# Optimization experiments

Measured on AMD Instinct MI355X. Metric: run time of the kernel, lower is better.

## Reference

```python
import jax, jax.numpy as jnp
import numpy as np

N_NODES = 200000
N_EDGES = 1600000
N_GRAPHS = 4096  # B*T = 256*16
FEATS = [5, 64, 128, 128]
H = 128


def setup_inputs() -> dict:
    key = jax.random.key(0)
    ks = jax.random.split(key, 32)
    inp = {
        "x": jax.random.normal(ks[0], (N_NODES, FEATS[0]), jnp.float32),
        "edge_attr": jax.random.uniform(ks[1], (N_EDGES,), jnp.float32),
        "edge_index": jax.random.randint(ks[2], (2, N_EDGES), 0, N_NODES),
        "batch_labels": jnp.sort(jax.random.randint(ks[3], (N_NODES,), 0, N_GRAPHS)),
        "label_map": jnp.arange(N_GRAPHS).reshape(256, 16),
    }
    ki = 4
    # GraphConv layers: self weight, neighbor weight, bias
    for li, (a, b) in enumerate(zip(FEATS[:-1], FEATS[1:])):
        s = (2.0 / a) ** 0.5
        inp[f"w_self{li}"] = jax.random.normal(ks[ki], (a, b), jnp.float32) * s; ki += 1
        inp[f"w_nei{li}"] = jax.random.normal(ks[ki], (a, b), jnp.float32) * s; ki += 1
        inp[f"b{li}"] = jnp.zeros((b,), jnp.float32)
    # GRU layers (PyTorch layout: W_ih [3H, in], W_hh [3H, H])
    for l in range(2):
        d_in = FEATS[-1] if l == 0 else H
        s = (1.0 / H) ** 0.5
        inp[f"wih{l}"] = jax.random.uniform(ks[ki], (3 * H, d_in), jnp.float32, -s, s); ki += 1
        inp[f"whh{l}"] = jax.random.uniform(ks[ki], (3 * H, H), jnp.float32, -s, s); ki += 1
        inp[f"bih{l}"] = jnp.zeros((3 * H,), jnp.float32)
        inp[f"bhh{l}"] = jnp.zeros((3 * H,), jnp.float32)
    inp["w_dec"] = jax.random.normal(ks[ki], (H, 1), jnp.float32) * (1.0 / H) ** 0.5; ki += 1
    inp["b_dec"] = jnp.zeros((1,), jnp.float32)
    return inp


def _gru_layer(seq, wih, whh, bih, bhh):
    # seq: [B, T, D] -> out [B, T, H], h_last [B, H]
    Hd = whh.shape[1]
    x_proj = seq @ wih.T + bih  # [B, T, 3H], precompute input projections

    def step(h_prev, xt):
        gh = h_prev @ whh.T + bhh
        xr, xz, xn = jnp.split(xt, 3, axis=-1)
        hr, hz, hn = jnp.split(gh, 3, axis=-1)
        r = jax.nn.sigmoid(xr + hr)
        z = jax.nn.sigmoid(xz + hz)
        n = jnp.tanh(xn + r * hn)
        h_new = (1.0 - z) * n + z * h_prev
        return h_new, h_new

    h0 = jnp.zeros((seq.shape[0], Hd), seq.dtype)
    h_last, outs = jax.lax.scan(step, h0, jnp.swapaxes(x_proj, 0, 1))
    return jnp.swapaxes(outs, 0, 1), h_last


def reference(x, edge_attr, w_self0, w_nei0, b0, w_self1, w_nei1, b1,
              w_self2, w_nei2, b2, wih0, whh0, bih0, bhh0, wih1, whh1,
              bih1, bhh1, w_dec, b_dec, edge_index, batch_labels, label_map):
    src, dst = edge_index[0], edge_index[1]
    n = x.shape[0]

    def conv(h, ws, wn, bb):
        # message = edge_weight * (W_nei h_src); aggregate by sum onto dst
        hn = h @ wn
        msg = hn[src] * edge_attr[:, None]  # [E, out]
        agg = jax.ops.segment_sum(msg, dst, num_segments=n)
        return jax.nn.relu(h @ ws + agg + bb)

    h = conv(x, w_self0, w_nei0, b0)
    h = conv(h, w_self1, w_nei1, b1)
    h = conv(h, w_self2, w_nei2, b2)

    # global_mean_pool over batch_labels
    sums = jax.ops.segment_sum(h, batch_labels, num_segments=N_GRAPHS)
    cnt = jax.ops.segment_sum(jnp.ones((n,), h.dtype), batch_labels, num_segments=N_GRAPHS)
    pooled = sums / jnp.maximum(cnt, 1.0)[:, None]  # [G, H]

    # group pooled graph embeddings into padded sequences [B, T, H]
    seq = pooled[label_map]

    o1, _ = _gru_layer(seq, wih0, whh0, bih0, bhh0)
    o2, h2 = _gru_layer(o1, wih1, whh1, bih1, bhh1)

    predictions = jax.nn.sigmoid(o2 @ w_dec + b_dec).squeeze(-1)  # [B, T]
    final_prediction = jax.nn.sigmoid(h2 @ w_dec + b_dec)  # [B, 1]
    return predictions, final_prediction
```

## Files before the change

### kernel.cpp

```cpp
#include <hip/hip_runtime.h>
#include <cmath>

typedef __attribute__((ext_vector_type(8))) short short8b;
typedef __attribute__((ext_vector_type(8))) unsigned short ushort8b;
typedef __attribute__((ext_vector_type(4))) float floatx4;

__device__ __forceinline__ float sigm(float x) { return 1.0f / (1.0f + expf(-x)); }

__device__ __forceinline__ unsigned short f2bf(float f) {
    unsigned u = __float_as_uint(f);
    unsigned r = (u + 0x7FFFu + ((u >> 16) & 1u)) >> 16;
    return (unsigned short)r;
}
__device__ __forceinline__ float bf2f(unsigned short b) {
    return __uint_as_float(((unsigned)b) << 16);
}

__global__ __launch_bounds__(512)
void bucket_hist(const int* __restrict__ dst, int* __restrict__ bcnt, int nE, int nBuck)
{
    __shared__ int h[512];
    const int t = threadIdx.x;
    h[t] = 0;
    __syncthreads();
    for (int i = blockIdx.x * 512 + t; i < nE; i += gridDim.x * 512)
        atomicAdd(&h[dst[i] >> 9], 1);
    __syncthreads();
    if (t < nBuck && h[t]) atomicAdd(&bcnt[t], h[t]);
}

__global__ __launch_bounds__(256)
void scan_blocks(const int* __restrict__ in, int* __restrict__ out,
                 int* __restrict__ bsum, int n)
{
    __shared__ int sh[256];
    int base = blockIdx.x * 1024;
    int t = threadIdx.x;
    int v[4];
    int s = 0;
    #pragma unroll
    for (int q = 0; q < 4; ++q) {
        int idx = base + t * 4 + q;
        v[q] = (idx < n) ? in[idx] : 0;
        s += v[q];
    }
    sh[t] = s;
    __syncthreads();
    for (int off = 1; off < 256; off <<= 1) {
        int x = (t >= off) ? sh[t - off] : 0;
        __syncthreads();
        sh[t] += x;
        __syncthreads();
    }
    int run = (t == 0) ? 0 : sh[t - 1];
    #pragma unroll
    for (int q = 0; q < 4; ++q) {
        int idx = base + t * 4 + q;
        if (idx < n) out[idx] = run;
        run += v[q];
    }
    if (t == 255 && bsum) bsum[blockIdx.x] = sh[255];
}

__global__ __launch_bounds__(512)
void bucket_scatter(const int* __restrict__ src, const int* __restrict__ dst,
                    const float* __restrict__ ea, int* __restrict__ bcur,
                    uint2* __restrict__ recs, int nE)
{
    __shared__ int hcnt[512];
    __shared__ int hbase[512];
    const int t = threadIdx.x;
    const int base = blockIdx.x * 8192;
    hcnt[t] = 0;
    __syncthreads();
    int eb[16], rank[16], dloc[16];
    #pragma unroll
    for (int q = 0; q < 16; ++q) {
        int e = base + q * 512 + t;
        if (e < nE) {
            int d = dst[e];
            eb[q] = d >> 9;
            dloc[q] = d & 511;
            rank[q] = atomicAdd(&hcnt[eb[q]], 1);
        }
    }
    __syncthreads();
    hbase[t] = hcnt[t] ? atomicAdd(&bcur[t], hcnt[t]) : 0;
    __syncthreads();
    #pragma unroll
    for (int q = 0; q < 16; ++q) {
        int e = base + q * 512 + t;
        if (e < nE) {
            int wq2 = __float2int_rn(ea[e] * 16383.f);
            uint2 r;
            r.x = (unsigned)((src[e] << 14) | wq2);
            r.y = (unsigned)dloc[q];
            recs[hbase[eb[q]] + rank[q]] = r;
        }
    }
}

__global__ __launch_bounds__(512)
void bucket_finalize(const uint2* __restrict__ recs, const int* __restrict__ boff,
                     int* __restrict__ rowptr, int* __restrict__ csr,
                     int nN, int nE, int nBuck)
{
    __shared__ int cnt[512];
    __shared__ int sc[512];
    __shared__ int cur[512];
    const int b = blockIdx.x;
    const int t = threadIdx.x;
    const int rbase = boff[b];
    const int rend  = (b + 1 < nBuck) ? boff[b + 1] : nE;
    const int rcnt  = rend - rbase;
    const int node0 = b << 9;
    const int nodes = min(512, nN - node0);
    cnt[t] = 0;
    __syncthreads();
    for (int i = t; i < rcnt; i += 512) atomicAdd(&cnt[recs[rbase + i].y], 1);
    __syncthreads();
    sc[t] = cnt[t];
    __syncthreads();
    for (int off = 1; off < 512; off <<= 1) {
        int v = (t >= off) ? sc[t - off] : 0;
        __syncthreads();
        sc[t] += v;
        __syncthreads();
    }
    int excl = (t == 0) ? 0 : sc[t - 1];
    if (t < nodes) rowptr[node0 + t] = rbase + excl;
    cur[t] = excl;
    __syncthreads();
    for (int i = t; i < rcnt; i += 512) {
        uint2 r = recs[rbase + i];
        int p = atomicAdd(&cur[r.y], 1);
        csr[rbase + p] = (int)r.x;
    }
}

__global__ __launch_bounds__(256)
void agg5_kernel(const float* __restrict__ x, const int* __restrict__ rowptr,
                 const int* __restrict__ csr, float* __restrict__ agg, int nN, int nE)
{
    int n = blockIdx.x * blockDim.x + threadIdx.x;
    if (n >= nN) return;
    int e0 = rowptr[n];
    int e1 = (n + 1 < nN) ? rowptr[n + 1] : nE;
    float a[5] = {0.f, 0.f, 0.f, 0.f, 0.f};
    for (int e = e0; e < e1; ++e) {
        int v = csr[e];
        int s = ((unsigned)v) >> 14;
        float w = (float)(v & 16383) * (1.f / 16383.f);
        const float* xr = x + (size_t)s * 5;
        #pragma unroll
        for (int f = 0; f < 5; ++f) a[f] += w * xr[f];
    }
    float* ar = agg + (size_t)n * 5;
    #pragma unroll
    for (int f = 0; f < 5; ++f) ar[f] = a[f];
}

template<int D>
__global__ __launch_bounds__(256)
void aggD_bf16(const unsigned short* __restrict__ h, const int* __restrict__ rowptr,
               const int* __restrict__ csr, unsigned short* __restrict__ agg,
               int nN, int nE)
{
    constexpr int TPN = D / 8;
    int gid = blockIdx.x * blockDim.x + threadIdx.x;
    int c = gid & (TPN - 1);
    int n = gid / TPN;
    if (n >= nN) return;
    int e0 = rowptr[n];
    int e1 = (n + 1 < nN) ? rowptr[n + 1] : nE;
    float acc[8] = {0.f, 0.f, 0.f, 0.f, 0.f, 0.f, 0.f, 0.f};
    int e = e0;
    for (; e + 3 < e1; e += 4) {
        int v0 = csr[e], v1 = csr[e + 1], v2 = csr[e + 2], v3 = csr[e + 3];
        const ushort8b h0 = *(const ushort8b*)(h + (size_t)(((unsigned)v0) >> 14) * D + c * 8);
        const ushort8b h1 = *(const ushort8b*)(h + (size_t)(((unsigned)v1) >> 14) * D + c * 8);
        const ushort8b h2 = *(const ushort8b*)(h + (size_t)(((unsigned)v2) >> 14) * D + c * 8);
        const ushort8b h3 = *(const ushort8b*)(h + (size_t)(((unsigned)v3) >> 14) * D + c * 8);
        float w0 = (float)(v0 & 16383) * (1.f / 16383.f);
        float w1 = (float)(v1 & 16383) * (1.f / 16383.f);
        float w2 = (float)(v2 & 16383) * (1.f / 16383.f);
        float w3 = (float)(v3 & 16383) * (1.f / 16383.f);
        #pragma unroll
        for (int q = 0; q < 8; ++q) {
            acc[q] += w0 * bf2f(h0[q]);
            acc[q] += w1 * bf2f(h1[q]);
            acc[q] += w2 * bf2f(h2[q]);
            acc[q] += w3 * bf2f(h3[q]);
        }
    }
    for (; e < e1; ++e) {
        int v = csr[e];
        int s = ((unsigned)v) >> 14;
        float w = (float)(v & 16383) * (1.f / 16383.f);
        const ushort8b hv = *(const ushort8b*)(h + (size_t)s * D + c * 8);
        #pragma unroll
        for (int q = 0; q < 8; ++q) acc[q] += w * bf2f(hv[q]);
    }
    ushort8b o;
    #pragma unroll
    for (int q = 0; q < 8; ++q) o[q] = f2bf(acc[q]);
    *(ushort8b*)(agg + (size_t)n * D + c * 8) = o;
}

template<int DIN, int DOUT>
__global__ __launch_bounds__(512)
void conv_mm(const float* __restrict__ h, const float* __restrict__ agg,
             const float* __restrict__ ws, const float* __restrict__ wn,
             const float* __restrict__ bias, unsigned short* __restrict__ out, int nN)
{
    __shared__ __align__(16) float s_w[2 * DIN * DOUT];
    __shared__ __align__(16) float s_b[DOUT];
    for (int i = threadIdx.x; i < DIN * DOUT; i += 512) {
        s_w[i] = ws[i];
        s_w[DIN * DOUT + i] = wn[i];
    }
    for (int i = threadIdx.x; i < DOUT; i += 512) s_b[i] = bias[i];
    __syncthreads();

    constexpr int TPN = DOUT / 4;
    constexpr int HALF = 512 / TPN;
    constexpr int NPASS = HALF * 2;
    const int jj = (threadIdx.x % TPN) * 4;
    const int nsub = threadIdx.x / TPN;

    for (int base = blockIdx.x * NPASS; base < nN; base += gridDim.x * NPASS) {
        int n0 = base + nsub;
        int n1 = base + nsub + HALF;
        bool v0 = n0 < nN, v1 = n1 < nN;
        int n0c = v0 ? n0 : nN - 1;
        int n1c = v1 ? n1 : nN - 1;

        float acc0[4], acc1[4];
        #pragma unroll
        for (int q = 0; q < 4; ++q) { acc0[q] = s_b[jj + q]; acc1[q] = s_b[jj + q]; }

        const float* p0 = h + (size_t)n0c * DIN;
        const float* p1 = h + (size_t)n1c * DIN;
        const float* a0 = agg + (size_t)n0c * DIN;
        const float* a1 = agg + (size_t)n1c * DIN;

        for (int k = 0; k < DIN; ++k) {
            float xs0 = p0[k], xs1 = p1[k];
            const float4 w4 = *(const float4*)(s_w + (size_t)k * DOUT + jj);
            acc0[0] += xs0 * w4.x; acc0[1] += xs0 * w4.y;
            acc0[2] += xs0 * w4.z; acc0[3] += xs0 * w4.w;
            acc1[0] += xs1 * w4.x; acc1[1] += xs1 * w4.y;
            acc1[2] += xs1 * w4.z; acc1[3] += xs1 * w4.w;
        }
        for (int k = 0; k < DIN; ++k) {
            float xs0 = a0[k], xs1 = a1[k];
            const float4 w4 = *(const float4*)(s_w + (size_t)(DIN + k) * DOUT + jj);
            acc0[0] += xs0 * w4.x; acc0[1] += xs0 * w4.y;
            acc0[2] += xs0 * w4.z; acc0[3] += xs0 * w4.w;
            acc1[0] += xs1 * w4.x; acc1[1] += xs1 * w4.y;
            acc1[2] += xs1 * w4.z; acc1[3] += xs1 * w4.w;
        }
        if (v0) {
            ushort4 o;
            o.x = f2bf(fmaxf(acc0[0], 0.f)); o.y = f2bf(fmaxf(acc0[1], 0.f));
            o.z = f2bf(fmaxf(acc0[2], 0.f)); o.w = f2bf(fmaxf(acc0[3], 0.f));
            *(ushort4*)(out + (size_t)n0 * DOUT + jj) = o;
        }
        if (v1) {
            ushort4 o;
            o.x = f2bf(fmaxf(acc1[0], 0.f)); o.y = f2bf(fmaxf(acc1[1], 0.f));
            o.z = f2bf(fmaxf(acc1[2], 0.f)); o.w = f2bf(fmaxf(acc1[3], 0.f));
            *(ushort4*)(out + (size_t)n1 * DOUT + jj) = o;
        }
    }
}

template<int DIN>
__global__ __launch_bounds__(256)
void prep_w(const float* __restrict__ ws, const float* __restrict__ wn,
            unsigned short* __restrict__ wt)
{
    constexpr int KC = 2 * DIN;
    int idx = blockIdx.x * 256 + threadIdx.x;
    if (idx >= 128 * KC) return;
    int col = idx / KC, k = idx % KC;
    float v = (k < DIN) ? ws[(size_t)k * 128 + col] : wn[(size_t)(k - DIN) * 128 + col];
    wt[(size_t)col * KC + k] = f2bf(v);
}

__global__ __launch_bounds__(256)
void prep_gru(const float* __restrict__ wih0, const float* __restrict__ whh0,
              const float* __restrict__ wih1, const float* __restrict__ whh1,
              unsigned short* __restrict__ wtx, unsigned short* __restrict__ wth)
{
    int i = blockIdx.x * 256 + threadIdx.x;
    if (i >= 384 * 128) return;
    wtx[i]             = f2bf(wih0[i]);
    wtx[384 * 128 + i] = f2bf(wih1[i]);
    wth[i]             = f2bf(whh0[i]);
    wth[384 * 128 + i] = f2bf(whh1[i]);
}

template<int DIN, bool POOL>
__global__ __launch_bounds__(256)
void conv_mfma(const unsigned short* __restrict__ h, const unsigned short* __restrict__ agg,
               const unsigned short* __restrict__ wt,
               const float* __restrict__ bias, unsigned short* __restrict__ out,
               const int* __restrict__ bl, float* __restrict__ sums, int nN)
{
    constexpr int KC = 2 * DIN;
    constexpr int NPANEL = KC / 64;
    constexpr int LDK = 72;
    constexpr int SMEM_BYTES = POOL ? 33280 : 27648;
    __shared__ __align__(16) unsigned char smem[SMEM_BYTES];
    unsigned short* sA = (unsigned short*)smem;
    unsigned short* sB = (unsigned short*)(smem + 9216);

    const int tid  = threadIdx.x;
    const int lane = tid & 63;
    const int w    = tid >> 6;
    const int nb   = (w >> 1) * 32;
    const int cb   = (w & 1) * 64;
    const int r15  = lane & 15;
    const int k8   = (lane >> 4) * 8;
    const int tile0 = blockIdx.x * 64;

    const floatx4 zero4 = {0.f, 0.f, 0.f, 0.f};
    floatx4 acc[2][4];
    #pragma unroll
    for (int m = 0; m < 2; ++m)
        #pragma unroll
        for (int n = 0; n < 4; ++n) acc[m][n] = zero4;

    for (int kp = 0; kp < NPANEL; ++kp) {
        const int kbase = kp * 64;
        const unsigned short* M = (kbase < DIN) ? h : agg;
        const int koff = (kbase < DIN) ? kbase : (kbase - DIN);
        #pragma unroll
        for (int r = 0; r < 2; ++r) {
            int f = tid + r * 256;
            int node = f >> 3, kq = f & 7;
            *(ushort8b*)(&sA[node * LDK + kq * 8]) =
                *(const ushort8b*)(M + (size_t)(tile0 + node) * DIN + koff + kq * 8);
        }
        #pragma unroll
        for (int r = 0; r < 4; ++r) {
            int f = tid + r * 256;
            int col = f >> 3, kq = f & 7;
            *(ushort8b*)(&sB[col * LDK + kq * 8]) =
                *(const ushort8b*)(wt + (size_t)col * KC + kbase + kq * 8);
        }
        __syncthreads();
        #pragma unroll
        for (int ks = 0; ks < 2; ++ks) {
            const int kk = ks * 32 + k8;
            short8b a0 = *(const short8b*)(&sA[(nb + r15) * LDK + kk]);
            short8b a1 = *(const short8b*)(&sA[(nb + 16 + r15) * LDK + kk]);
            #pragma unroll
            for (int n = 0; n < 4; ++n) {
                short8b b = *(const short8b*)(&sB[(cb + n * 16 + r15) * LDK + kk]);
                acc[0][n] = __builtin_amdgcn_mfma_f32_16x16x32_bf16(a0, b, acc[0][n], 0, 0, 0);
                acc[1][n] = __builtin_amdgcn_mfma_f32_16x16x32_bf16(a1, b, acc[1][n], 0, 0, 0);
            }
        }
        __syncthreads();
    }

    const int row4 = (lane >> 4) * 4;
    if constexpr (POOL) {
        float* s_out = (float*)smem;
        int*   s_gl  = (int*)(smem + 33024);
        #pragma unroll
        for (int n = 0; n < 4; ++n) {
            const int col = cb + n * 16 + r15;
            const float bv = bias[col];
            #pragma unroll
            for (int m = 0; m < 2; ++m) {
                #pragma unroll
                for (int j = 0; j < 4; ++j) {
                    int row = nb + m * 16 + row4 + j;
                    s_out[row * 129 + col] = fmaxf(acc[m][n][j] + bv, 0.f);
                }
            }
        }
        if (tid < 64) s_gl[tid] = bl[tile0 + tid];
        __syncthreads();
        {
            const int col  = tid & 127;
            const int r0   = (tid >> 7) * 32;
            float run = 0.f;
            int gprev = s_gl[r0];
            for (int r = r0; r < r0 + 32; ++r) {
                int g = s_gl[r];
                float v = s_out[r * 129 + col];
                if (g != gprev) {
                    unsafeAtomicAdd(&sums[(size_t)gprev * 128 + col], run);
                    run = v;
                    gprev = g;
                } else {
                    run += v;
                }
            }
            unsafeAtomicAdd(&sums[(size_t)gprev * 128 + col], run);
        }
    } else {
        #pragma unroll
        for (int n = 0; n < 4; ++n) {
            const int col = cb + n * 16 + r15;
            const float bv = bias[col];
            #pragma unroll
            for (int m = 0; m < 2; ++m) {
                #pragma unroll
                for (int j = 0; j < 4; ++j) {
                    int node = tile0 + nb + m * 16 + row4 + j;
                    out[(size_t)node * 128 + col] = f2bf(fmaxf(acc[m][n][j] + bv, 0.f));
                }
            }
        }
    }
}

__global__ __launch_bounds__(256)
void cnt_bs(const int* __restrict__ bl, float* __restrict__ cnt, int nN, int nG)
{
    int g = blockIdx.x * blockDim.x + threadIdx.x;
    if (g >= nG) return;
    int lo = 0, hi = nN;
    while (lo < hi) { int mid = (lo + hi) >> 1; if (bl[mid] < g) lo = mid + 1; else hi = mid; }
    int s = lo;
    hi = nN;
    while (lo < hi) { int mid = (lo + hi) >> 1; if (bl[mid] < g + 1) lo = mid + 1; else hi = mid; }
    cnt[g] = (float)(lo - s);
}

__global__ __launch_bounds__(256)
void xproj_kernel(const float* __restrict__ sums, const float* __restrict__ cnt,
                  const int* __restrict__ lmap, const unsigned short* __restrict__ wx0,
                  const float* __restrict__ bih0, float* __restrict__ xp, int nRows)
{
    __shared__ __align__(16) unsigned short s_a[32 * 136];
    __shared__ float s_b[384];
    const int tid  = threadIdx.x;
    const int lane = tid & 63;
    const int w    = tid >> 6;
    const int r15  = lane & 15;
    const int k8   = (lane >> 4) * 8;
    const int row4 = (lane >> 4) * 4;
    const int base = blockIdx.x * 32;

    for (int i = tid; i < 32 * 128; i += 256) {
        int row = i >> 7, j = i & 127;
        int g = lmap[base + row];
        float v = sums[(size_t)g * 128 + j] / fmaxf(cnt[g], 1.f);
        s_a[row * 136 + j] = f2bf(v);
    }
    for (int i = tid; i < 384; i += 256) s_b[i] = bih0[i];
    __syncthreads();

    const int rt = (w & 1) * 16;
    const int cg = (w >> 1) * 192;
    const floatx4 zero4 = {0.f, 0.f, 0.f, 0.f};
    floatx4 acc[12];
    #pragma unroll
    for (int ct = 0; ct < 12; ++ct) acc[ct] = zero4;

    #pragma unroll
    for (int kk = 0; kk < 4; ++kk) {
        short8b a = *(const short8b*)(&s_a[(rt + r15) * 136 + kk * 32 + k8]);
        #pragma unroll
        for (int ct = 0; ct < 12; ++ct) {
            int col = cg + ct * 16 + r15;
            short8b b = *(const short8b*)(wx0 + (size_t)col * 128 + kk * 32 + k8);
            acc[ct] = __builtin_amdgcn_mfma_f32_16x16x32_bf16(a, b, acc[ct], 0, 0, 0);
        }
    }
    #pragma unroll
    for (int ct = 0; ct < 12; ++ct) {
        int col = cg + ct * 16 + r15;
        float bv = s_b[col];
        #pragma unroll
        for (int j = 0; j < 4; ++j) {
            int R = base + rt + row4 + j;
            xp[(size_t)R * 384 + col] = acc[ct][j] + bv;
        }
    }
}

__global__ __launch_bounds__(384)
void gru_rec(const float* __restrict__ xp0,
             const unsigned short* __restrict__ wgx,
             const unsigned short* __restrict__ wgh,
             const float* __restrict__ bhh0, const float* __restrict__ bih1,
             const float* __restrict__ bhh1,
             const float* __restrict__ wdec, const float* __restrict__ bdec,
             float* __restrict__ out, int nG)
{
    constexpr int SLD = 136;
    __shared__ float s_xp[16 * 384];
    __shared__ __align__(16) unsigned short s_o[16 * SLD];
    __shared__ __align__(16) unsigned short s_hb[128];
    __shared__ float s_hf[128];
    __shared__ float s_gh[384];
    __shared__ float s_bhh[2][384];
    __shared__ float s_bih1[384];
    __shared__ float s_wdec[128];

    const int b    = blockIdx.x;
    const int tid  = threadIdx.x;
    const int lane = tid & 63;
    const int w    = tid >> 6;
    const int r15  = lane & 15;
    const int k8   = (lane >> 4) * 8;
    const int row4 = (lane >> 4) * 4;
    const int cbase = w * 64;
    const floatx4 zero4 = {0.f, 0.f, 0.f, 0.f};

    for (int i = tid; i < 16 * 384; i += 384)
        s_xp[i] = xp0[(size_t)b * 16 * 384 + i];
    s_bhh[0][tid] = bhh0[tid];
    s_bhh[1][tid] = bhh1[tid];
    s_bih1[tid]   = bih1[tid];
    if (tid < 128) { s_wdec[tid] = wdec[tid]; s_hf[tid] = 0.f; s_hb[tid] = 0; }

    short8b bf[4][4];
    {
        const unsigned short* W = wgh;
        #pragma unroll
        for (int ct = 0; ct < 4; ++ct) {
            int col = cbase + ct * 16 + r15;
            #pragma unroll
            for (int kk = 0; kk < 4; ++kk)
                bf[ct][kk] = *(const short8b*)(W + (size_t)col * 128 + kk * 32 + k8);
        }
    }
    __syncthreads();

    for (int t = 0; t < 16; ++t) {
        floatx4 acc[4] = {zero4, zero4, zero4, zero4};
        #pragma unroll
        for (int kk = 0; kk < 4; ++kk) {
            short8b a = *(const short8b*)(&s_hb[kk * 32 + k8]);
            #pragma unroll
            for (int ct = 0; ct < 4; ++ct)
                acc[ct] = __builtin_amdgcn_mfma_f32_16x16x32_bf16(a, bf[ct][kk], acc[ct], 0, 0, 0);
        }
        if (lane < 16) {
            #pragma unroll
            for (int ct = 0; ct < 4; ++ct) {
                int col = cbase + ct * 16 + lane;
                s_gh[col] = acc[ct][0] + s_bhh[0][col];
            }
        }
        __syncthreads();
        if (tid < 128) {
            const float* xr = &s_xp[t * 384];
            float r = sigm(xr[tid] + s_gh[tid]);
            float z = sigm(xr[128 + tid] + s_gh[128 + tid]);
            float n = tanhf(xr[256 + tid] + r * s_gh[256 + tid]);
            float hv = (1.f - z) * n + z * s_hf[tid];
            s_hf[tid] = hv;
            unsigned short hb = f2bf(hv);
            s_hb[tid] = hb;
            s_o[t * SLD + tid] = hb;
        }
        __syncthreads();
    }

    {
        const unsigned short* W1 = wgx + (size_t)384 * 128;
        #pragma unroll
        for (int ct = 0; ct < 4; ++ct) {
            int col = cbase + ct * 16 + r15;
            #pragma unroll
            for (int kk = 0; kk < 4; ++kk)
                bf[ct][kk] = *(const short8b*)(W1 + (size_t)col * 128 + kk * 32 + k8);
        }
        floatx4 acc[4] = {zero4, zero4, zero4, zero4};
        #pragma unroll
        for (int kk = 0; kk < 4; ++kk) {
            short8b a = *(const short8b*)(&s_o[r15 * SLD + kk * 32 + k8]);
            #pragma unroll
            for (int ct = 0; ct < 4; ++ct)
                acc[ct] = __builtin_amdgcn_mfma_f32_16x16x32_bf16(a, bf[ct][kk], acc[ct], 0, 0, 0);
        }
        #pragma unroll
        for (int ct = 0; ct < 4; ++ct) {
            int col = cbase + ct * 16 + r15;
            float bv = s_bih1[col];
            #pragma unroll
            for (int j = 0; j < 4; ++j) {
                int t = row4 + j;
                s_xp[t * 384 + col] = acc[ct][j] + bv;
            }
        }
    }
    {
        const unsigned short* W = wgh + (size_t)384 * 128;
        #pragma unroll
        for (int ct = 0; ct < 4; ++ct) {
            int col = cbase + ct * 16 + r15;
            #pragma unroll
            for (int kk = 0; kk < 4; ++kk)
                bf[ct][kk] = *(const short8b*)(W + (size_t)col * 128 + kk * 32 + k8);
        }
    }
    if (tid < 128) { s_hf[tid] = 0.f; s_hb[tid] = 0; }
    __syncthreads();

    for (int t = 0; t < 16; ++t) {
        floatx4 acc[4] = {zero4, zero4, zero4, zero4};
        #pragma unroll
        for (int kk = 0; kk < 4; ++kk) {
            short8b a = *(const short8b*)(&s_hb[kk * 32 + k8]);
            #pragma unroll
            for (int ct = 0; ct < 4; ++ct)
                acc[ct] = __builtin_amdgcn_mfma_f32_16x16x32_bf16(a, bf[ct][kk], acc[ct], 0, 0, 0);
        }
        if (lane < 16) {
            #pragma unroll
            for (int ct = 0; ct < 4; ++ct) {
                int col = cbase + ct * 16 + lane;
                s_gh[col] = acc[ct][0] + s_bhh[1][col];
            }
        }
        __syncthreads();
        if (tid < 128) {
            const float* xr = &s_xp[t * 384];
            float r = sigm(xr[tid] + s_gh[tid]);
            float z = sigm(xr[128 + tid] + s_gh[128 + tid]);
            float n = tanhf(xr[256 + tid] + r * s_gh[256 + tid]);
            float hv = (1.f - z) * n + z * s_hf[tid];
            s_hf[tid] = hv;
            unsigned short hb = f2bf(hv);
            s_hb[tid] = hb;
            s_o[t * SLD + tid] = hb;
        }
        __syncthreads();
    }

    if (tid < 16) {
        float acc = bdec[0];
        const unsigned short* row = &s_o[tid * SLD];
        #pragma unroll 16
        for (int k = 0; k < 128; ++k) acc += bf2f(row[k]) * s_wdec[k];
        float p = sigm(acc);
        out[b * 16 + tid] = p;
        if (tid == 15) out[nG + b] = p;
    }
}

extern "C" void kernel_launch(void* const* d_in, const int* in_sizes, int n_in,
                              void* d_out, int out_size, void* d_ws, size_t ws_size,
                              hipStream_t stream)
{
    const float* x    = (const float*)d_in[0];
    const float* ea   = (const float*)d_in[1];
    const int*   ei   = (const int*)d_in[2];
    const int*   bl   = (const int*)d_in[3];
    const int*   lmap = (const int*)d_in[4];
    const float* ws0 = (const float*)d_in[5];
    const float* wn0 = (const float*)d_in[6];
    const float* b0  = (const float*)d_in[7];
    const float* ws1 = (const float*)d_in[8];
    const float* wn1 = (const float*)d_in[9];
    const float* b1  = (const float*)d_in[10];
    const float* ws2 = (const float*)d_in[11];
    const float* wn2 = (const float*)d_in[12];
    const float* b2  = (const float*)d_in[13];
    const float* wih0 = (const float*)d_in[14];
    const float* whh0 = (const float*)d_in[15];
    const float* bih0 = (const float*)d_in[16];
    const float* bhh0 = (const float*)d_in[17];
    const float* wih1 = (const float*)d_in[18];
    const float* whh1 = (const float*)d_in[19];
    const float* bih1 = (const float*)d_in[20];
    const float* bhh1 = (const float*)d_in[21];
    const float* wdec = (const float*)d_in[22];
    const float* bdec = (const float*)d_in[23];
    float* out = (float*)d_out;

    const int nN = in_sizes[0] / 5;
    const int nE = in_sizes[1];
    const int nG = in_sizes[4];
    const int B  = nG / 16;
    const int nBuck = (nN + 511) >> 9;

    const int* src = ei;
    const int* dst = ei + nE;

    unsigned short* R0   = (unsigned short*)d_ws;
    unsigned short* R1   = R0 + (size_t)nN * 64;
    unsigned short* R2   = R1 + (size_t)nN * 64;
    unsigned short* agg128b = R0;
    float* agg5 = (float*)(R2 + (size_t)nN * 128);
    float* sums = agg5 + (size_t)nN * 5;
    float* cnt  = sums + (size_t)nG * 128;
    int* rowptr = (int*)(cnt + nG);
    int* bcnt   = rowptr + nN;
    int* boff   = bcnt + 512;
    int* bcur   = boff + 512;
    uint2* recs = (uint2*)(bcur + 512);
    int* csr    = (int*)(recs + nE);
    unsigned short* wt1 = (unsigned short*)(csr + nE);
    unsigned short* wt2 = wt1 + 128 * 128;
    unsigned short* wgx = wt2 + 128 * 256;
    unsigned short* wgh = wgx + 2 * 384 * 128;
    float* xp0 = (float*)(wgh + 2 * 384 * 128);

    hipMemsetAsync(bcnt, 0, 512 * sizeof(int), stream);
    bucket_hist<<<256, 512, 0, stream>>>(dst, bcnt, nE, nBuck);
    scan_blocks<<<1, 256, 0, stream>>>(bcnt, boff, nullptr, nBuck);
    hipMemcpyAsync(bcur, boff, nBuck * sizeof(int), hipMemcpyDeviceToDevice, stream);
    bucket_scatter<<<(nE + 8191) / 8192, 512, 0, stream>>>(src, dst, ea, bcur, recs, nE);
    bucket_finalize<<<nBuck, 512, 0, stream>>>(recs, boff, rowptr, csr, nN, nE, nBuck);

    prep_w<64><<<(128 * 128 + 255) / 256, 256, 0, stream>>>(ws1, wn1, wt1);
    prep_w<128><<<(128 * 256 + 255) / 256, 256, 0, stream>>>(ws2, wn2, wt2);
    prep_gru<<<(384 * 128 + 255) / 256, 256, 0, stream>>>(wih0, whh0, wih1, whh1, wgx, wgh);

    agg5_kernel<<<(nN + 255) / 256, 256, 0, stream>>>(x, rowptr, csr, agg5, nN, nE);
    conv_mm<5, 64><<<512, 512, 0, stream>>>(x, agg5, ws0, wn0, b0, R0, nN);

    aggD_bf16<64><<<(nN * 8 + 255) / 256, 256, 0, stream>>>(R0, rowptr, csr, R1, nN, nE);
    conv_mfma<64, false><<<nN / 64, 256, 0, stream>>>(R0, R1, wt1, b1, R2, nullptr, nullptr, nN);

    aggD_bf16<128><<<(nN * 16 + 255) / 256, 256, 0, stream>>>(R2, rowptr, csr, agg128b, nN, nE);
    hipMemsetAsync(sums, 0, (size_t)nG * 128 * sizeof(float), stream);
    cnt_bs<<<(nG + 255) / 256, 256, 0, stream>>>(bl, cnt, nN, nG);
    conv_mfma<128, true><<<nN / 64, 256, 0, stream>>>(R2, agg128b, wt2, b2, nullptr, bl, sums, nN);

    xproj_kernel<<<nG / 32, 256, 0, stream>>>(sums, cnt, lmap, wgx, bih0, xp0, nG);
    gru_rec<<<B, 384, 0, stream>>>(xp0, wgx, wgh, bhh0, bih1, bhh1, wdec, bdec, out, nG);
}
```

Baseline: 306.6 us.

## Fuse neighbor aggregation into MFMA conv kernel via shared-memory tile

The separate aggD_bf16 gather kernels are removed. Each conv block now aggregates its own 64 nodes' neighbor features into a shared-memory tile and feeds the agg half of the K dimension to the MFMAs straight from that tile. This avoids writing and re-reading the aggregated bf16 matrix through global memory and saves two kernel launches. In exchange, shared memory per block grows and the latency-bound gather now sits inside the GEMM kernel, which may reduce occupancy and overlap.

```diff
diff --git a/kernel.cpp b/kernel.cpp
--- a/kernel.cpp
+++ b/kernel.cpp
@@ -160,53 +160,6 @@
     for (int f = 0; f < 5; ++f) ar[f] = a[f];
 }
 
-template<int D>
-__global__ __launch_bounds__(256)
-void aggD_bf16(const unsigned short* __restrict__ h, const int* __restrict__ rowptr,
-               const int* __restrict__ csr, unsigned short* __restrict__ agg,
-               int nN, int nE)
-{
-    constexpr int TPN = D / 8;
-    int gid = blockIdx.x * blockDim.x + threadIdx.x;
-    int c = gid & (TPN - 1);
-    int n = gid / TPN;
-    if (n >= nN) return;
-    int e0 = rowptr[n];
-    int e1 = (n + 1 < nN) ? rowptr[n + 1] : nE;
-    float acc[8] = {0.f, 0.f, 0.f, 0.f, 0.f, 0.f, 0.f, 0.f};
-    int e = e0;
-    for (; e + 3 < e1; e += 4) {
-        int v0 = csr[e], v1 = csr[e + 1], v2 = csr[e + 2], v3 = csr[e + 3];
-        const ushort8b h0 = *(const ushort8b*)(h + (size_t)(((unsigned)v0) >> 14) * D + c * 8);
-        const ushort8b h1 = *(const ushort8b*)(h + (size_t)(((unsigned)v1) >> 14) * D + c * 8);
-        const ushort8b h2 = *(const ushort8b*)(h + (size_t)(((unsigned)v2) >> 14) * D + c * 8);
-        const ushort8b h3 = *(const ushort8b*)(h + (size_t)(((unsigned)v3) >> 14) * D + c * 8);
-        float w0 = (float)(v0 & 16383) * (1.f / 16383.f);
-        float w1 = (float)(v1 & 16383) * (1.f / 16383.f);
-        float w2 = (float)(v2 & 16383) * (1.f / 16383.f);
-        float w3 = (float)(v3 & 16383) * (1.f / 16383.f);
-        #pragma unroll
-        for (int q = 0; q < 8; ++q) {
-            acc[q] += w0 * bf2f(h0[q]);
-            acc[q] += w1 * bf2f(h1[q]);
-            acc[q] += w2 * bf2f(h2[q]);
-            acc[q] += w3 * bf2f(h3[q]);
-        }
-    }
-    for (; e < e1; ++e) {
-        int v = csr[e];
-        int s = ((unsigned)v) >> 14;
-        float w = (float)(v & 16383) * (1.f / 16383.f);
-        const ushort8b hv = *(const ushort8b*)(h + (size_t)s * D + c * 8);
-        #pragma unroll
-        for (int q = 0; q < 8; ++q) acc[q] += w * bf2f(hv[q]);
-    }
-    ushort8b o;
-    #pragma unroll
-    for (int q = 0; q < 8; ++q) o[q] = f2bf(acc[q]);
-    *(ushort8b*)(agg + (size_t)n * D + c * 8) = o;
-}
-
 template<int DIN, int DOUT>
 __global__ __launch_bounds__(512)
 void conv_mm(const float* __restrict__ h, const float* __restrict__ agg,
@@ -303,18 +256,23 @@
 
 template<int DIN, bool POOL>
 __global__ __launch_bounds__(256)
-void conv_mfma(const unsigned short* __restrict__ h, const unsigned short* __restrict__ agg,
-               const unsigned short* __restrict__ wt,
-               const float* __restrict__ bias, unsigned short* __restrict__ out,
-               const int* __restrict__ bl, float* __restrict__ sums, int nN)
+void conv_fused(const unsigned short* __restrict__ h,
+                const int* __restrict__ rowptr, const int* __restrict__ csr,
+                const unsigned short* __restrict__ wt,
+                const float* __restrict__ bias, unsigned short* __restrict__ out,
+                const int* __restrict__ bl, float* __restrict__ sums,
+                int nN, int nE)
 {
     constexpr int KC = 2 * DIN;
     constexpr int NPANEL = KC / 64;
     constexpr int LDK = 72;
-    constexpr int SMEM_BYTES = POOL ? 33280 : 27648;
+    constexpr int ALD = DIN + 8;
+    constexpr int BASE_BYTES = 9216 + 18432;
+    constexpr int SMEM_BYTES = BASE_BYTES + 64 * ALD * 2;
     __shared__ __align__(16) unsigned char smem[SMEM_BYTES];
-    unsigned short* sA = (unsigned short*)smem;
-    unsigned short* sB = (unsigned short*)(smem + 9216);
+    unsigned short* sA   = (unsigned short*)smem;
+    unsigned short* sB   = (unsigned short*)(smem + 9216);
+    unsigned short* sAgg = (unsigned short*)(smem + BASE_BYTES);
 
     const int tid  = threadIdx.x;
     const int lane = tid & 63;
@@ -325,6 +283,53 @@
     const int k8   = (lane >> 4) * 8;
     const int tile0 = blockIdx.x * 64;
 
+    {
+        constexpr int TPN = DIN / 8;
+        constexpr int GRP = 256 / TPN;
+        constexpr int NPT = 64 / GRP;
+        const int c  = tid & (TPN - 1);
+        const int n0 = tid / TPN;
+        #pragma unroll
+        for (int it = 0; it < NPT; ++it) {
+            int node = n0 + it * GRP;
+            int gn = tile0 + node;
+            int e0 = rowptr[gn];
+            int e1 = (gn + 1 < nN) ? rowptr[gn + 1] : nE;
+            float acc[8] = {0.f, 0.f, 0.f, 0.f, 0.f, 0.f, 0.f, 0.f};
+            int e = e0;
+            for (; e + 3 < e1; e += 4) {
+                int v0 = csr[e], v1 = csr[e + 1], v2 = csr[e + 2], v3 = csr[e + 3];
+                const ushort8b h0 = *(const ushort8b*)(h + (size_t)(((unsigned)v0) >> 14) * DIN + c * 8);
+                const ushort8b h1 = *(const ushort8b*)(h + (size_t)(((unsigned)v1) >> 14) * DIN + c * 8);
+                const ushort8b h2 = *(const ushort8b*)(h + (size_t)(((unsigned)v2) >> 14) * DIN + c * 8);
+                const ushort8b h3 = *(const ushort8b*)(h + (size_t)(((unsigned)v3) >> 14) * DIN + c * 8);
+                float w0 = (float)(v0 & 16383) * (1.f / 16383.f);
+                float w1 = (float)(v1 & 16383) * (1.f / 16383.f);
+                float w2 = (float)(v2 & 16383) * (1.f / 16383.f);
+                float w3 = (float)(v3 & 16383) * (1.f / 16383.f);
+                #pragma unroll
+                for (int q = 0; q < 8; ++q) {
+                    acc[q] += w0 * bf2f(h0[q]);
+                    acc[q] += w1 * bf2f(h1[q]);
+                    acc[q] += w2 * bf2f(h2[q]);
+                    acc[q] += w3 * bf2f(h3[q]);
+                }
+            }
+            for (; e < e1; ++e) {
+                int v = csr[e];
+                float wv = (float)(v & 16383) * (1.f / 16383.f);
+                const ushort8b hv = *(const ushort8b*)(h + (size_t)(((unsigned)v) >> 14) * DIN + c * 8);
+                #pragma unroll
+                for (int q = 0; q < 8; ++q) acc[q] += wv * bf2f(hv[q]);
+            }
+            ushort8b o;
+            #pragma unroll
+            for (int q = 0; q < 8; ++q) o[q] = f2bf(acc[q]);
+            *(ushort8b*)(&sAgg[node * ALD + c * 8]) = o;
+        }
+    }
+    __syncthreads();
+
     const floatx4 zero4 = {0.f, 0.f, 0.f, 0.f};
     floatx4 acc[2][4];
     #pragma unroll
@@ -334,14 +339,15 @@
 
     for (int kp = 0; kp < NPANEL; ++kp) {
         const int kbase = kp * 64;
-        const unsigned short* M = (kbase < DIN) ? h : agg;
-        const int koff = (kbase < DIN) ? kbase : (kbase - DIN);
-        #pragma unroll
-        for (int r = 0; r < 2; ++r) {
-            int f = tid + r * 256;
-            int node = f >> 3, kq = f & 7;
-            *(ushort8b*)(&sA[node * LDK + kq * 8]) =
-                *(const ushort8b*)(M + (size_t)(tile0 + node) * DIN + koff + kq * 8);
+        const bool isH = (kbase < DIN);
+        if (isH) {
+            #pragma unroll
+            for (int r = 0; r < 2; ++r) {
+                int f = tid + r * 256;
+                int node = f >> 3, kq = f & 7;
+                *(ushort8b*)(&sA[node * LDK + kq * 8]) =
+                    *(const ushort8b*)(h + (size_t)(tile0 + node) * DIN + kbase + kq * 8);
+            }
         }
         #pragma unroll
         for (int r = 0; r < 4; ++r) {
@@ -351,11 +357,18 @@
                 *(const ushort8b*)(wt + (size_t)col * KC + kbase + kq * 8);
         }
         __syncthreads();
+        const int koff = kbase - DIN;
         #pragma unroll
         for (int ks = 0; ks < 2; ++ks) {
             const int kk = ks * 32 + k8;
-            short8b a0 = *(const short8b*)(&sA[(nb + r15) * LDK + kk]);
-            short8b a1 = *(const short8b*)(&sA[(nb + 16 + r15) * LDK + kk]);
+            short8b a0, a1;
+            if (isH) {
+                a0 = *(const short8b*)(&sA[(nb + r15) * LDK + kk]);
+                a1 = *(const short8b*)(&sA[(nb + 16 + r15) * LDK + kk]);
+            } else {
+                a0 = *(const short8b*)(&sAgg[(nb + r15) * ALD + koff + kk]);
+                a1 = *(const short8b*)(&sAgg[(nb + 16 + r15) * ALD + koff + kk]);
+            }
             #pragma unroll
             for (int n = 0; n < 4; ++n) {
                 short8b b = *(const short8b*)(&sB[(cb + n * 16 + r15) * LDK + kk]);
@@ -691,7 +704,6 @@
     unsigned short* R0   = (unsigned short*)d_ws;
     unsigned short* R1   = R0 + (size_t)nN * 64;
     unsigned short* R2   = R1 + (size_t)nN * 64;
-    unsigned short* agg128b = R0;
     float* agg5 = (float*)(R2 + (size_t)nN * 128);
     float* sums = agg5 + (size_t)nN * 5;
     float* cnt  = sums + (size_t)nG * 128;
@@ -721,13 +733,13 @@
     agg5_kernel<<<(nN + 255) / 256, 256, 0, stream>>>(x, rowptr, csr, agg5, nN, nE);
     conv_mm<5, 64><<<512, 512, 0, stream>>>(x, agg5, ws0, wn0, b0, R0, nN);
 
-    aggD_bf16<64><<<(nN * 8 + 255) / 256, 256, 0, stream>>>(R0, rowptr, csr, R1, nN, nE);
-    conv_mfma<64, false><<<nN / 64, 256, 0, stream>>>(R0, R1, wt1, b1, R2, nullptr, nullptr, nN);
-
-    aggD_bf16<128><<<(nN * 16 + 255) / 256, 256, 0, stream>>>(R2, rowptr, csr, agg128b, nN, nE);
+    conv_fused<64, false><<<nN / 64, 256, 0, stream>>>(R0, rowptr, csr, wt1, b1, R2,
+                                                       nullptr, nullptr, nN, nE);
+
     hipMemsetAsync(sums, 0, (size_t)nG * 128 * sizeof(float), stream);
     cnt_bs<<<(nG + 255) / 256, 256, 0, stream>>>(bl, cnt, nN, nG);
-    conv_mfma<128, true><<<nN / 64, 256, 0, stream>>>(R2, agg128b, wt2, b2, nullptr, bl, sums, nN);
+    conv_fused<128, true><<<nN / 64, 256, 0, stream>>>(R2, rowptr, csr, wt2, b2, nullptr,
+                                                       bl, sums, nN, nE);
 
     xproj_kernel<<<nG / 32, 256, 0, stream>>>(sums, cnt, lmap, wgx, bih0, xp0, nG);
     gru_rec<<<B, 384, 0, stream>>>(xp0, wgx, wgh, bhh0, bih1, bhh1, wdec, bdec, out, nG);
```

New measurement: 333.9 us. 1.09x slower.
